# Performance work log

Hardware: AMD Instinct MI355X
Metric: run time of the kernel (lower is better)

The kernel has to match this reference:

```python
import jax, jax.numpy as jnp
import numpy as np

N = 100000      # spots (nodes)
E = 1600000     # directed edges
D_IN = 1000     # genes
ALPHA = 0.9
BN_EPS = 1e-3   # BatchNorm(momentum=0.01, eps=0.001), eval mode


def _bn(x, g, b, m, v):
    # eval-mode batchnorm with running stats
    return (x - m) * jax.lax.rsqrt(v + BN_EPS) * g + b


def _gcn(h, row, col, w, b):
    # PyG GCNConv: h' = D^-1/2 (A + I) D^-1/2 (h W) + b
    n = h.shape[0]
    h = h @ w
    ones = jnp.ones((row.shape[0],), h.dtype)
    deg = jnp.ones((n,), h.dtype).at[col].add(ones)  # degree incl. self-loop
    dinv = jax.lax.rsqrt(deg)
    msg = h[row] * (dinv[row] * dinv[col])[:, None]   # gather + edge norm
    agg = jnp.zeros_like(h).at[col].add(msg)          # scatter-add
    agg = agg + h * (1.0 / deg)[:, None]              # self-loop term
    return agg + b


def setup_inputs() -> dict:
    key = jax.random.key(0)
    ks = iter(jax.random.split(key, 48))
    f32 = jnp.float32

    def glorot(shape):
        return jax.random.normal(next(ks), shape, f32) * np.float32(1.0 / np.sqrt(shape[0]))

    def bnp(n):
        g = jax.random.uniform(next(ks), (n,), f32, 0.9, 1.1)
        b = jax.random.normal(next(ks), (n,), f32) * 0.1
        m = jax.random.normal(next(ks), (n,), f32) * 0.1
        v = jax.random.uniform(next(ks), (n,), f32, 0.5, 1.5)
        return g, b, m, v

    inp = {}
    inp['x'] = jax.random.normal(next(ks), (N, D_IN), f32)
    inp['edge_index'] = jax.random.randint(next(ks), (2, E), 0, N, jnp.int64)
    # encoder L0: 1000 -> 256
    inp['enc0_w'] = glorot((D_IN, 256)); inp['enc0_b'] = jnp.zeros((256,), f32)
    inp['enc0_g'], inp['enc0_bb'], inp['enc0_m'], inp['enc0_v'] = bnp(256)
    # encoder L1: 256 -> 64
    inp['enc1_w'] = glorot((256, 64)); inp['enc1_b'] = jnp.zeros((64,), f32)
    inp['enc1_g'], inp['enc1_bb'], inp['enc1_m'], inp['enc1_v'] = bnp(64)
    # GCN: 64 -> 128 (conv_hidden[0]*2)
    inp['conv_w'] = glorot((64, 128)); inp['conv_b'] = jnp.zeros((128,), f32)
    inp['conv_g'], inp['conv_bb'], inp['conv_m'], inp['conv_v'] = bnp(128)
    # GCN mean / logvar heads: 128 -> 16
    inp['mean_w'] = glorot((128, 16)); inp['mean_b'] = jnp.zeros((16,), f32)
    inp['logvar_w'] = glorot((128, 16)); inp['logvar_b'] = jnp.zeros((16,), f32)
    # decoder L0: 80 -> 64
    inp['dec0_w'] = glorot((80, 64)); inp['dec0_b'] = jnp.zeros((64,), f32)
    inp['dec0_g'], inp['dec0_bb'], inp['dec0_m'], inp['dec0_v'] = bnp(64)
    # decoder L1: 64 -> 1000
    inp['dec1_w'] = glorot((64, D_IN)); inp['dec1_b'] = jnp.zeros((D_IN,), f32)
    # cluster layer [15, 80]
    inp['cluster'] = jax.random.normal(next(ks), (15, 80), f32) * np.float32(np.sqrt(2.0 / (15 + 80)))
    return inp


def reference(x, edge_index, enc0_w, enc0_b, enc0_g, enc0_bb, enc0_m, enc0_v,
              enc1_w, enc1_b, enc1_g, enc1_bb, enc1_m, enc1_v,
              conv_w, conv_b, conv_g, conv_bb, conv_m, conv_v,
              mean_w, mean_b, logvar_w, logvar_b,
              dec0_w, dec0_b, dec0_g, dec0_bb, dec0_m, dec0_v,
              dec1_w, dec1_b, cluster):
    row, col = edge_index[0], edge_index[1]
    # linear encoder (Linear + BN(eval) + ELU; dropout off in eval)
    h = jax.nn.elu(_bn(x @ enc0_w + enc0_b, enc0_g, enc0_bb, enc0_m, enc0_v))
    feat_x = jax.nn.elu(_bn(h @ enc1_w + enc1_b, enc1_g, enc1_bb, enc1_m, enc1_v))
    # graph encoder
    c = jax.nn.relu(_bn(_gcn(feat_x, row, col, conv_w, conv_b), conv_g, conv_bb, conv_m, conv_v))
    mu = _gcn(c, row, col, mean_w, mean_b)
    logvar = _gcn(c, row, col, logvar_w, logvar_b)
    gnn_z = mu  # reparameterize in eval mode returns mu
    z = jnp.concatenate([feat_x, gnn_z], axis=1)  # [N, 80]
    # decoder
    d = jax.nn.elu(_bn(z @ dec0_w + dec0_b, dec0_g, dec0_bb, dec0_m, dec0_v))
    de_feat = d @ dec1_w + dec1_b
    # student-t cluster soft assignment (||z-c||^2 via expansion, no [N,K,80] tensor)
    dist = jnp.maximum(jnp.sum(z * z, 1, keepdims=True)
                       + jnp.sum(cluster * cluster, 1)[None, :]
                       - 2.0 * (z @ cluster.T), 0.0)
    q = 1.0 / (1.0 + dist / ALPHA + 1e-8)
    q = q ** ((ALPHA + 1.0) / 2.0)
    q = q / jnp.sum(q, 1, keepdims=True)
    return (z, mu, logvar, de_feat, q, feat_x, gnn_z)
```

## Files before the change

kernel.cpp:

```cpp
#include <hip/hip_runtime.h>
#include <hip/hip_bf16.h>

#define NN 100000
#define NE 1600000
#define DIN 1000
#define BN_EPS 1e-3f
#define NB 391

#define OZ  ((size_t)0)
#define OMU ((size_t)NN*80)
#define OLV ((size_t)NN*96)
#define ODE ((size_t)NN*112)
#define OQ  ((size_t)NN*1112)
#define OFX ((size_t)NN*1127)
#define OGZ ((size_t)NN*1191)

typedef __attribute__((ext_vector_type(8))) short short8v;
typedef __attribute__((ext_vector_type(4))) short short4v;
typedef __attribute__((ext_vector_type(4))) float f32x4;

__device__ __forceinline__ float elu_f(float x) { return x > 0.f ? x : expf(x) - 1.f; }

__device__ __forceinline__ short f2bf(float f) {
    union { float f; unsigned u; } c; c.f = f;
    unsigned r = c.u + 0x7fffu + ((c.u >> 16) & 1u);
    return (short)(r >> 16);
}
__device__ __forceinline__ float b2f(short s) {
    union { unsigned u; float f; } c; c.u = ((unsigned)(unsigned short)s) << 16; return c.f;
}
__device__ __forceinline__ float b2f_lo(unsigned p) {
    union { unsigned u; float f; } c; c.u = p << 16; return c.f;
}
__device__ __forceinline__ float b2f_hi(unsigned p) {
    union { unsigned u; float f; } c; c.u = p & 0xffff0000u; return c.f;
}

__device__ __forceinline__ int edge_at(const void* ei, int is64, size_t idx) {
    if (is64) return (int)((const long long*)ei)[idx];
    return ((const int*)ei)[idx];
}

__global__ __launch_bounds__(256) void k_detect(const int* __restrict__ ei, int* __restrict__ flag) {
    __shared__ int nz;
    if (threadIdx.x == 0) nz = 0;
    __syncthreads();
    for (int i = threadIdx.x; i < 2048; i += 256)
        if (ei[2 * i + 1] != 0) nz = 1;
    __syncthreads();
    if (threadIdx.x == 0) flag[0] = (nz == 0) ? 1 : 0;
}

__global__ __launch_bounds__(256) void k_deg_init(float* __restrict__ deg) {
    int i = blockIdx.x * 256 + threadIdx.x;
    if (i < NN) deg[i] = 1.0f;
}

__global__ __launch_bounds__(256) void k_deg_accum(const void* __restrict__ ei, const int* __restrict__ flag,
                                                   float* __restrict__ deg) {
    const int is64 = flag[0];
    int e = blockIdx.x * 256 + threadIdx.x;
    if (e < NE) atomicAdd(&deg[edge_at(ei, is64, (size_t)NE + e)], 1.0f);
}

__global__ __launch_bounds__(256) void k_scan1(const float* __restrict__ deg, int* __restrict__ off,
                                               int* __restrict__ bsum, int* __restrict__ cursor) {
    __shared__ int s[256];
    const int t = threadIdx.x;
    const int i = blockIdx.x * 256 + t;
    const int vv = (i < NN) ? ((int)deg[i]) - 1 : 0;
    if (i < NN) cursor[i] = 0;
    s[t] = vv;
    __syncthreads();
    for (int d = 1; d < 256; d <<= 1) {
        const int u = (t >= d) ? s[t - d] : 0;
        __syncthreads();
        s[t] += u;
        __syncthreads();
    }
    if (i < NN) off[i] = s[t] - vv;
    if (t == 255) bsum[blockIdx.x] = s[t];
}

__global__ __launch_bounds__(512) void k_scan2(int* __restrict__ bsum) {
    __shared__ int s[512];
    const int t = threadIdx.x;
    const int vv = (t < NB) ? bsum[t] : 0;
    s[t] = vv;
    __syncthreads();
    for (int d = 1; d < 512; d <<= 1) {
        const int u = (t >= d) ? s[t - d] : 0;
        __syncthreads();
        s[t] += u;
        __syncthreads();
    }
    if (t < NB) bsum[t] = s[t] - vv;
}

__global__ __launch_bounds__(256) void k_scan3(int* __restrict__ off, const int* __restrict__ bsum) {
    const int i = blockIdx.x * 256 + threadIdx.x;
    if (i < NN) off[i] += bsum[blockIdx.x];
}

__global__ __launch_bounds__(256) void k_fill(const void* __restrict__ ei, const int* __restrict__ flag,
                                              const float* __restrict__ deg, const int* __restrict__ off,
                                              int* __restrict__ cursor, int2* __restrict__ csr_e) {
    const int is64 = flag[0];
    const int e = blockIdx.x * 256 + threadIdx.x;
    if (e >= NE) return;
    const int r = edge_at(ei, is64, e);
    const int c = edge_at(ei, is64, (size_t)NE + e);
    const float w = rsqrtf(deg[r]) * rsqrtf(deg[c]);
    const int p = atomicAdd(&cursor[c], 1);
    csr_e[off[c] + p] = make_int2(r, __float_as_int(w));
}

__global__ __launch_bounds__(256) void k_wt(const float* __restrict__ w, short* __restrict__ wt) {
    const int tid = blockIdx.x * 256 + threadIdx.x;
    const int c = tid >> 10;
    const int k = tid & 1023;
    wt[((size_t)(k >> 3) * 256 + c) * 8 + (k & 7)] = (k < DIN) ? f2bf(w[(size_t)k * 256 + c]) : (short)0;
}

__global__ __launch_bounds__(256) void k_wt2(const float* __restrict__ w, short* __restrict__ wt2) {
    const int tid = blockIdx.x * 256 + threadIdx.x;
    const int c = tid >> 6;
    const int k = tid & 63;
    wt2[(size_t)c * 64 + k] = (c < DIN) ? f2bf(w[(size_t)k * DIN + c]) : (short)0;
}

__global__ __launch_bounds__(512, 2) void k_enc0_mfma(
    const float* __restrict__ x, const short* __restrict__ wt, const float* __restrict__ bias,
    const float* __restrict__ g, const float* __restrict__ bb,
    const float* __restrict__ m, const float* __restrict__ v,
    short* __restrict__ h1bf)
{
    __shared__ short As[4 * 128 * 8];
    __shared__ short Bs[4 * 256 * 8];
    const int t = threadIdx.x;
    const int lane = t & 63;
    const int wave = t >> 6;
    const int wm = (wave >> 2) * 64;
    const int wn = (wave & 3) * 64;
    const int row0 = blockIdx.x * 128;

    f32x4 acc[4][4];
    #pragma unroll
    for (int mi = 0; mi < 4; ++mi)
        #pragma unroll
        for (int ni = 0; ni < 4; ++ni)
            acc[mi][ni] = (f32x4){0.f, 0.f, 0.f, 0.f};

    const int kq = t & 7;
    const int rA0 = t >> 3;
    const int rA1 = rA0 + 64;
    const int gr0 = (row0 + rA0 < NN) ? (row0 + rA0) : (NN - 1);
    const int gr1 = (row0 + rA1 < NN) ? (row0 + rA1) : (NN - 1);
    const float* xb0 = x + (size_t)gr0 * DIN;
    const float* xb1 = x + (size_t)gr1 * DIN;
    short4v* aslot0 = reinterpret_cast<short4v*>(&As[(((kq >> 1) * 128) + rA0) * 8 + (kq & 1) * 4]);
    short4v* aslot1 = reinterpret_cast<short4v*>(&As[(((kq >> 1) * 128) + rA1) * 8 + (kq & 1) * 4]);

    const int colB = t & 255;
    const int kcB0 = t >> 8;
    const int kcB1 = 2 + (t >> 8);

    const int kc = lane >> 4;
    const int lr = lane & 15;

    float4 pf0 = *reinterpret_cast<const float4*>(xb0 + kq * 4);
    float4 pf1 = *reinterpret_cast<const float4*>(xb1 + kq * 4);

    for (int ks = 0; ks < 32; ++ks) {
        __syncthreads();
        {
            const int kb = ks * 32 + kq * 4;
            short4v p0, p1;
            if (kb + 4 <= DIN) {
                p0[0] = f2bf(pf0.x); p0[1] = f2bf(pf0.y); p0[2] = f2bf(pf0.z); p0[3] = f2bf(pf0.w);
                p1[0] = f2bf(pf1.x); p1[1] = f2bf(pf1.y); p1[2] = f2bf(pf1.z); p1[3] = f2bf(pf1.w);
            } else {
                p0 = (short4v){0, 0, 0, 0};
                p1 = (short4v){0, 0, 0, 0};
            }
            *aslot0 = p0;
            *aslot1 = p1;
        }
        {
            const int gbase = ks * 4;
            *reinterpret_cast<short8v*>(&Bs[((size_t)kcB0 * 256 + colB) * 8]) =
                *reinterpret_cast<const short8v*>(&wt[((size_t)(gbase + kcB0) * 256 + colB) * 8]);
            *reinterpret_cast<short8v*>(&Bs[((size_t)kcB1 * 256 + colB) * 8]) =
                *reinterpret_cast<const short8v*>(&wt[((size_t)(gbase + kcB1) * 256 + colB) * 8]);
        }
        if (ks + 1 < 32) {
            const int kb2 = (ks + 1) * 32 + kq * 4;
            const int ko = (kb2 + 4 <= DIN) ? kb2 : 0;
            pf0 = *reinterpret_cast<const float4*>(xb0 + ko);
            pf1 = *reinterpret_cast<const float4*>(xb1 + ko);
        }
        __syncthreads();
        short8v a[4], b[4];
        #pragma unroll
        for (int mi = 0; mi < 4; ++mi)
            a[mi] = *reinterpret_cast<const short8v*>(&As[((size_t)kc * 128 + wm + mi * 16 + lr) * 8]);
        #pragma unroll
        for (int ni = 0; ni < 4; ++ni)
            b[ni] = *reinterpret_cast<const short8v*>(&Bs[((size_t)kc * 256 + wn + ni * 16 + lr) * 8]);
        #pragma unroll
        for (int mi = 0; mi < 4; ++mi)
            #pragma unroll
            for (int ni = 0; ni < 4; ++ni)
                acc[mi][ni] = __builtin_amdgcn_mfma_f32_16x16x32_bf16(a[mi], b[ni], acc[mi][ni], 0, 0, 0);
    }

    float sc[4], sh[4];
    int cols[4];
    #pragma unroll
    for (int ni = 0; ni < 4; ++ni) {
        const int col = wn + ni * 16 + lr;
        cols[ni] = col;
        const float s = rsqrtf(v[col] + BN_EPS) * g[col];
        sc[ni] = s;
        sh[ni] = (bias[col] - m[col]) * s + bb[col];
    }
    #pragma unroll
    for (int mi = 0; mi < 4; ++mi) {
        #pragma unroll
        for (int j = 0; j < 4; ++j) {
            const int row = row0 + wm + mi * 16 + (lane >> 4) * 4 + j;
            if (row < NN) {
                #pragma unroll
                for (int ni = 0; ni < 4; ++ni) {
                    const float y = acc[mi][ni][j] * sc[ni] + sh[ni];
                    h1bf[(size_t)row * 256 + cols[ni]] = f2bf(elu_f(y));
                }
            }
        }
    }
}

__global__ __launch_bounds__(256) void k_enc1(
    const short* __restrict__ h1bf, const float* __restrict__ w, const float* __restrict__ bias,
    const float* __restrict__ g, const float* __restrict__ bb,
    const float* __restrict__ m, const float* __restrict__ v,
    float* __restrict__ feat, short* __restrict__ featbf, float* __restrict__ out)
{
    __shared__ short hs[32 * 256];
    const int t = threadIdx.x;
    const int row0 = blockIdx.x * 32;
    const int j0 = t & 31;
    const int r0 = (t >> 5) * 4;
    float acc[4][2] = {};
    for (int idx = t; idx < 1024; idx += 256) {
        const int r = idx >> 5, c8 = idx & 31;
        *reinterpret_cast<short8v*>(&hs[r * 256 + c8 * 8]) =
            *reinterpret_cast<const short8v*>(&h1bf[(size_t)(row0 + r) * 256 + c8 * 8]);
    }
    __syncthreads();
    #pragma unroll 1
    for (int k = 0; k < 256; k += 8) {
        float wv[8][2];
        #pragma unroll
        for (int kk = 0; kk < 8; ++kk) {
            wv[kk][0] = w[(k + kk) * 64 + j0];
            wv[kk][1] = w[(k + kk) * 64 + j0 + 32];
        }
        #pragma unroll
        for (int r = 0; r < 4; ++r) {
            const short8v hv = *reinterpret_cast<const short8v*>(&hs[(r0 + r) * 256 + k]);
            #pragma unroll
            for (int kk = 0; kk < 8; ++kk) {
                const float xa = b2f(hv[kk]);
                acc[r][0] = fmaf(xa, wv[kk][0], acc[r][0]);
                acc[r][1] = fmaf(xa, wv[kk][1], acc[r][1]);
            }
        }
    }
    #pragma unroll
    for (int c = 0; c < 2; ++c) {
        const int j = j0 + 32 * c;
        const float sc = rsqrtf(v[j] + BN_EPS) * g[j];
        const float sh = (bias[j] - m[j]) * sc + bb[j];
        #pragma unroll
        for (int r = 0; r < 4; ++r) {
            const size_t rowi = row0 + r0 + r;
            const float y = elu_f(acc[r][c] * sc + sh);
            feat[rowi * 64 + j] = y;
            featbf[rowi * 64 + j] = f2bf(y);
            out[OFX + rowi * 64 + j] = y;
            out[OZ + rowi * 80 + j] = y;
        }
    }
}

__global__ __launch_bounds__(256) void k_feat_gather(
    const unsigned* __restrict__ featp, const float* __restrict__ deg,
    const int* __restrict__ off, const int2* __restrict__ csr_e,
    float* __restrict__ aggF)
{
    const int t = threadIdx.x;
    const int node = blockIdx.x * 8 + (t >> 5);
    const int lane = t & 31;
    const float dg = deg[node];
    const float dinv = 1.0f / dg;
    const unsigned ps = featp[(size_t)node * 32 + lane];
    float a0 = b2f_lo(ps) * dinv;
    float a1 = b2f_hi(ps) * dinv;
    const int beg = off[node];
    const int end = beg + ((int)dg - 1);
    for (int s = beg; s < end; ++s) {
        const int2 e = csr_e[s];
        const float w = __int_as_float(e.y);
        const unsigned p = featp[(size_t)e.x * 32 + lane];
        a0 = fmaf(b2f_lo(p), w, a0);
        a1 = fmaf(b2f_hi(p), w, a1);
    }
    float2 o; o.x = a0; o.y = a1;
    *reinterpret_cast<float2*>(&aggF[(size_t)node * 64 + lane * 2]) = o;
}

__global__ __launch_bounds__(256) void k_conv_mlp_proj(
    const float* __restrict__ aggF, const float* __restrict__ w, const float* __restrict__ cb,
    const float* __restrict__ g, const float* __restrict__ bb,
    const float* __restrict__ m, const float* __restrict__ v,
    const float* __restrict__ mw, const float* __restrict__ lw,
    short* __restrict__ m2bf)
{
    __shared__ float fs[32 * 64];
    __shared__ float cs[32 * 128];
    const int t = threadIdx.x;
    const int row0 = blockIdx.x * 32;
    {
        const int j0 = t & 63;
        const int r0 = (t >> 6) * 8;
        float acc[8][2] = {};
        for (int idx = t; idx < 512; idx += 256) {
            const int r = idx >> 4, c4 = idx & 15;
            *reinterpret_cast<float4*>(&fs[r * 64 + c4 * 4]) =
                *reinterpret_cast<const float4*>(&aggF[(size_t)(row0 + r) * 64 + c4 * 4]);
        }
        __syncthreads();
        #pragma unroll 1
        for (int k = 0; k < 64; k += 4) {
            float wv[4][2];
            #pragma unroll
            for (int kk = 0; kk < 4; ++kk) {
                wv[kk][0] = w[(k + kk) * 128 + j0];
                wv[kk][1] = w[(k + kk) * 128 + j0 + 64];
            }
            #pragma unroll
            for (int r = 0; r < 8; ++r) {
                const float4 xv = *reinterpret_cast<const float4*>(&fs[(r0 + r) * 64 + k]);
                const float xa[4] = {xv.x, xv.y, xv.z, xv.w};
                #pragma unroll
                for (int kk = 0; kk < 4; ++kk) {
                    acc[r][0] = fmaf(xa[kk], wv[kk][0], acc[r][0]);
                    acc[r][1] = fmaf(xa[kk], wv[kk][1], acc[r][1]);
                }
            }
        }
        #pragma unroll
        for (int c = 0; c < 2; ++c) {
            const int j = j0 + 64 * c;
            const float sc = rsqrtf(v[j] + BN_EPS) * g[j];
            const float sh = bb[j] - m[j] * sc;
            const float cbj = cb[j];
            #pragma unroll
            for (int r = 0; r < 8; ++r) {
                const float val = acc[r][c] + cbj;
                cs[(r0 + r) * 128 + j] = fmaxf(fmaf(val, sc, sh), 0.f);
            }
        }
    }
    __syncthreads();
    {
        const int j0 = t & 15;
        const int r0 = (t >> 4) * 2;
        float acc[2][2] = {};
        #pragma unroll 1
        for (int k = 0; k < 128; k += 4) {
            float wv[4][2];
            #pragma unroll
            for (int kk = 0; kk < 4; ++kk) {
                wv[kk][0] = mw[(k + kk) * 16 + j0];
                wv[kk][1] = lw[(k + kk) * 16 + j0];
            }
            #pragma unroll
            for (int r = 0; r < 2; ++r) {
                const float4 xv = *reinterpret_cast<const float4*>(&cs[(r0 + r) * 128 + k]);
                const float xa[4] = {xv.x, xv.y, xv.z, xv.w};
                #pragma unroll
                for (int kk = 0; kk < 4; ++kk) {
                    acc[r][0] = fmaf(xa[kk], wv[kk][0], acc[r][0]);
                    acc[r][1] = fmaf(xa[kk], wv[kk][1], acc[r][1]);
                }
            }
        }
        #pragma unroll
        for (int r = 0; r < 2; ++r) {
            const size_t rowi = row0 + r0 + r;
            m2bf[rowi * 32 + j0] = f2bf(acc[r][0]);
            m2bf[rowi * 32 + 16 + j0] = f2bf(acc[r][1]);
        }
    }
}

__global__ __launch_bounds__(256) void k_mlp_gather(
    const unsigned* __restrict__ m2p, const float* __restrict__ deg,
    const int* __restrict__ off, const int2* __restrict__ csr_e,
    const float* __restrict__ mb, const float* __restrict__ lb,
    float* __restrict__ agg2)
{
    const int t = threadIdx.x;
    const int node = blockIdx.x * 16 + (t >> 4);
    const int lane = t & 15;
    const int f0 = lane * 2, f1 = lane * 2 + 1;
    const float dg = deg[node];
    const float dinv = 1.0f / dg;
    const float b0 = (f0 < 16) ? mb[f0] : lb[f0 - 16];
    const float b1 = (f1 < 16) ? mb[f1] : lb[f1 - 16];
    const unsigned ps = m2p[(size_t)node * 16 + lane];
    float a0 = fmaf(b2f_lo(ps), dinv, b0);
    float a1 = fmaf(b2f_hi(ps), dinv, b1);
    const int beg = off[node];
    const int end = beg + ((int)dg - 1);
    for (int s = beg; s < end; ++s) {
        const int2 e = csr_e[s];
        const float w = __int_as_float(e.y);
        const unsigned p = m2p[(size_t)e.x * 16 + lane];
        a0 = fmaf(b2f_lo(p), w, a0);
        a1 = fmaf(b2f_hi(p), w, a1);
    }
    float2 o; o.x = a0; o.y = a1;
    *reinterpret_cast<float2*>(&agg2[(size_t)node * 32 + lane * 2]) = o;
}

__global__ __launch_bounds__(256) void k_final_pre(
    const float* __restrict__ feat, const float* __restrict__ agg2,
    const float* __restrict__ d0w, const float* __restrict__ d0b,
    const float* __restrict__ g, const float* __restrict__ bb,
    const float* __restrict__ m, const float* __restrict__ v,
    const float* __restrict__ cluster,
    short* __restrict__ d0bf,
    float* __restrict__ out)
{
    __shared__ float zs[8][80];
    __shared__ float qs[8][15];
    const int t = threadIdx.x;
    const int row0 = blockIdx.x * 8;

    for (int idx = t; idx < 512; idx += 256) {
        const int r = idx >> 6, k = idx & 63;
        zs[r][k] = feat[(size_t)(row0 + r) * 64 + k];
    }
    if (t < 128) {
        const int r = t >> 4, k = t & 15;
        const size_t rowi = row0 + r;
        const float muv = agg2[rowi * 32 + k];
        const float lv = agg2[rowi * 32 + 16 + k];
        zs[r][64 + k] = muv;
        out[OMU + rowi * 16 + k] = muv;
        out[OGZ + rowi * 16 + k] = muv;
        out[OZ + rowi * 80 + 64 + k] = muv;
        out[OLV + rowi * 16 + k] = lv;
    }
    __syncthreads();

    for (int idx = t; idx < 512; idx += 256) {
        const int r = idx >> 6, n = idx & 63;
        float acc = 0.f;
        #pragma unroll
        for (int k = 0; k < 80; k += 4) {
            const float4 zv = *reinterpret_cast<const float4*>(&zs[r][k]);
            acc = fmaf(zv.x, d0w[(k + 0) * 64 + n], acc);
            acc = fmaf(zv.y, d0w[(k + 1) * 64 + n], acc);
            acc = fmaf(zv.z, d0w[(k + 2) * 64 + n], acc);
            acc = fmaf(zv.w, d0w[(k + 3) * 64 + n], acc);
        }
        acc += d0b[n];
        const float sc = rsqrtf(v[n] + BN_EPS) * g[n];
        const float y = elu_f((acc - m[n]) * sc + bb[n]);
        d0bf[(size_t)(row0 + r) * 64 + n] = f2bf(y);
    }

    if (t < 120) {
        const int r = t / 15, c = t % 15;
        float zz = 0.f, cc = 0.f, dot = 0.f;
        #pragma unroll 1
        for (int k = 0; k < 80; ++k) {
            const float zv = zs[r][k];
            const float cv = cluster[c * 80 + k];
            zz = fmaf(zv, zv, zz);
            cc = fmaf(cv, cv, cc);
            dot = fmaf(zv, cv, dot);
        }
        const float dist = fmaxf(zz + cc - 2.f * dot, 0.f);
        qs[r][c] = powf(1.0f / (1.0f + dist / 0.9f + 1e-8f), 0.95f);
    }
    __syncthreads();
    if (t < 120) {
        const int r = t / 15, c = t % 15;
        float s = 0.f;
        #pragma unroll
        for (int c2 = 0; c2 < 15; ++c2) s += qs[r][c2];
        out[OQ + (size_t)(row0 + r) * 15 + c] = qs[r][c] / s;
    }
}

__global__ __launch_bounds__(256) void k_dec1_mfma(
    const short* __restrict__ d0bf, const short* __restrict__ wt2,
    const float* __restrict__ d1b, float* __restrict__ out)
{
    const int t = threadIdx.x;
    const int lane = t & 63;
    const int wave = t >> 6;
    const int wm = (wave >> 1) * 64;
    const int wn = (wave & 1) * 64;
    const int row0 = blockIdx.x * 128;
    const int col0 = blockIdx.y * 128;
    const int kc = lane >> 4;
    const int lr = lane & 15;

    f32x4 acc[4][4];
    #pragma unroll
    for (int mi = 0; mi < 4; ++mi)
        #pragma unroll
        for (int ni = 0; ni < 4; ++ni)
            acc[mi][ni] = (f32x4){0.f, 0.f, 0.f, 0.f};

    #pragma unroll
    for (int ks = 0; ks < 2; ++ks) {
        const int k0 = ks * 32 + kc * 8;
        short8v a[4], b[4];
        #pragma unroll
        for (int mi = 0; mi < 4; ++mi) {
            const int row = row0 + wm + mi * 16 + lr;
            if (row < NN)
                a[mi] = *reinterpret_cast<const short8v*>(&d0bf[(size_t)row * 64 + k0]);
            else
                a[mi] = (short8v){0, 0, 0, 0, 0, 0, 0, 0};
        }
        #pragma unroll
        for (int ni = 0; ni < 4; ++ni) {
            const int col = col0 + wn + ni * 16 + lr;
            b[ni] = *reinterpret_cast<const short8v*>(&wt2[(size_t)col * 64 + k0]);
        }
        #pragma unroll
        for (int mi = 0; mi < 4; ++mi)
            #pragma unroll
            for (int ni = 0; ni < 4; ++ni)
                acc[mi][ni] = __builtin_amdgcn_mfma_f32_16x16x32_bf16(a[mi], b[ni], acc[mi][ni], 0, 0, 0);
    }

    #pragma unroll
    for (int ni = 0; ni < 4; ++ni) {
        const int col = col0 + wn + ni * 16 + lr;
        if (col < DIN) {
            const float bv = d1b[col];
            #pragma unroll
            for (int mi = 0; mi < 4; ++mi) {
                #pragma unroll
                for (int j = 0; j < 4; ++j) {
                    const int row = row0 + wm + mi * 16 + (lane >> 4) * 4 + j;
                    if (row < NN)
                        out[ODE + (size_t)row * DIN + col] = acc[mi][ni][j] + bv;
                }
            }
        }
    }
}

extern "C" void kernel_launch(void* const* d_in, const int* in_sizes, int n_in,
                              void* d_out, int out_size, void* d_ws, size_t ws_size,
                              hipStream_t stream)
{
    const float* x       = (const float*)d_in[0];
    const void*  ei      = d_in[1];
    const float* enc0_w  = (const float*)d_in[2];
    const float* enc0_b  = (const float*)d_in[3];
    const float* enc0_g  = (const float*)d_in[4];
    const float* enc0_bb = (const float*)d_in[5];
    const float* enc0_m  = (const float*)d_in[6];
    const float* enc0_v  = (const float*)d_in[7];
    const float* enc1_w  = (const float*)d_in[8];
    const float* enc1_b  = (const float*)d_in[9];
    const float* enc1_g  = (const float*)d_in[10];
    const float* enc1_bb = (const float*)d_in[11];
    const float* enc1_m  = (const float*)d_in[12];
    const float* enc1_v  = (const float*)d_in[13];
    const float* conv_w  = (const float*)d_in[14];
    const float* conv_b  = (const float*)d_in[15];
    const float* conv_g  = (const float*)d_in[16];
    const float* conv_bb = (const float*)d_in[17];
    const float* conv_m  = (const float*)d_in[18];
    const float* conv_v  = (const float*)d_in[19];
    const float* mean_w  = (const float*)d_in[20];
    const float* mean_b  = (const float*)d_in[21];
    const float* logvar_w = (const float*)d_in[22];
    const float* logvar_b = (const float*)d_in[23];
    const float* dec0_w  = (const float*)d_in[24];
    const float* dec0_b  = (const float*)d_in[25];
    const float* dec0_g  = (const float*)d_in[26];
    const float* dec0_bb = (const float*)d_in[27];
    const float* dec0_m  = (const float*)d_in[28];
    const float* dec0_v  = (const float*)d_in[29];
    const float* dec1_w  = (const float*)d_in[30];
    const float* dec1_b  = (const float*)d_in[31];
    const float* cluster = (const float*)d_in[32];

    float* ws = (float*)d_ws;
    float* deg  = ws;
    float* feat = ws + NN;
    float* A    = ws + (size_t)65 * NN;
    size_t base = (size_t)321 * NN;
    int*   off     = (int*)(ws + base);
    int*   cursor  = (int*)(ws + base + NN);
    int*   bsum    = (int*)(ws + base + 2 * (size_t)NN);
    int2*  csr_e   = (int2*)(ws + base + 2 * (size_t)NN + 512);
    short* wt      = (short*)(ws + base + 2 * (size_t)NN + 512 + 2 * (size_t)NE);
    int*   flag    = (int*)(ws + base + 2 * (size_t)NN + 512 + 2 * (size_t)NE + 131072);

    short* h1bf   = (short*)A;
    short* featbf = (short*)(A + (size_t)128 * NN);
    float* aggF   = A;
    short* m2bf   = (short*)(A + (size_t)128 * NN);
    float* agg2   = A + (size_t)32 * NN;
    short* d0bf   = (short*)(A + (size_t)64 * NN);
    short* wt2    = wt;

    float* out = (float*)d_out;

    k_detect<<<1, 256, 0, stream>>>((const int*)ei, flag);
    k_deg_init<<<NB, 256, 0, stream>>>(deg);
    k_deg_accum<<<NE / 256, 256, 0, stream>>>(ei, flag, deg);

    k_scan1<<<NB, 256, 0, stream>>>(deg, off, bsum, cursor);
    k_scan2<<<1, 512, 0, stream>>>(bsum);
    k_scan3<<<NB, 256, 0, stream>>>(off, bsum);
    k_fill<<<NE / 256, 256, 0, stream>>>(ei, flag, deg, off, cursor, csr_e);

    k_wt<<<1024, 256, 0, stream>>>(enc0_w, wt);
    k_enc0_mfma<<<(NN + 127) / 128, 512, 0, stream>>>(x, wt, enc0_b, enc0_g, enc0_bb, enc0_m, enc0_v, h1bf);
    k_wt2<<<256, 256, 0, stream>>>(dec1_w, wt2);

    k_enc1<<<NN / 32, 256, 0, stream>>>(h1bf, enc1_w, enc1_b, enc1_g, enc1_bb, enc1_m, enc1_v,
                                        feat, featbf, out);

    k_feat_gather<<<NN / 8, 256, 0, stream>>>((const unsigned*)featbf, deg, off, csr_e, aggF);
    k_conv_mlp_proj<<<NN / 32, 256, 0, stream>>>(aggF, conv_w, conv_b,
                                                 conv_g, conv_bb, conv_m, conv_v,
                                                 mean_w, logvar_w, m2bf);

    k_mlp_gather<<<NN / 16, 256, 0, stream>>>((const unsigned*)m2bf, deg, off, csr_e,
                                              mean_b, logvar_b, agg2);

    k_final_pre<<<NN / 8, 256, 0, stream>>>(feat, agg2, dec0_w, dec0_b, dec0_g, dec0_bb, dec0_m, dec0_v,
                                            cluster, d0bf, out);
    {
        dim3 grid((NN + 127) / 128, 8);
        k_dec1_mfma<<<grid, 256, 0, stream>>>(d0bf, wt2, dec1_b, out);
    }
}
```

Before: 1.053 ms.

## Double-buffer LDS tiles in encoder GEMM to overlap loads with MFMA

The encoder-0 bf16 MFMA GEMM now uses two LDS buffers for the A and B tiles. Global loads for the next K step, including the weight tile, are issued before the current step's MFMAs, and the results are written to the alternate buffer afterward, so only one barrier per iteration is needed. This is meant to hide global-memory latency behind compute and to remove one sync per K step. In exchange it doubles shared memory use (from 24KB to 48KB per block), which could limit occupancy at two blocks per CU, and it raises register pressure from the held prefetch values.

```diff
diff --git a/kernel.cpp b/kernel.cpp
--- a/kernel.cpp
+++ b/kernel.cpp
@@ -135,8 +135,8 @@
     const float* __restrict__ m, const float* __restrict__ v,
     short* __restrict__ h1bf)
 {
-    __shared__ short As[4 * 128 * 8];
-    __shared__ short Bs[4 * 256 * 8];
+    __shared__ short As[2][4 * 128 * 8];
+    __shared__ short Bs[2][4 * 256 * 8];
     const int t = threadIdx.x;
     const int lane = t & 63;
     const int wave = t >> 6;
@@ -158,60 +158,77 @@
     const int gr1 = (row0 + rA1 < NN) ? (row0 + rA1) : (NN - 1);
     const float* xb0 = x + (size_t)gr0 * DIN;
     const float* xb1 = x + (size_t)gr1 * DIN;
-    short4v* aslot0 = reinterpret_cast<short4v*>(&As[(((kq >> 1) * 128) + rA0) * 8 + (kq & 1) * 4]);
-    short4v* aslot1 = reinterpret_cast<short4v*>(&As[(((kq >> 1) * 128) + rA1) * 8 + (kq & 1) * 4]);
+    const size_t aoff0 = (((kq >> 1) * 128) + rA0) * 8 + (kq & 1) * 4;
+    const size_t aoff1 = (((kq >> 1) * 128) + rA1) * 8 + (kq & 1) * 4;
 
     const int colB = t & 255;
     const int kcB0 = t >> 8;
     const int kcB1 = 2 + (t >> 8);
+    const size_t boff0 = ((size_t)kcB0 * 256 + colB) * 8;
+    const size_t boff1 = ((size_t)kcB1 * 256 + colB) * 8;
 
     const int kc = lane >> 4;
     const int lr = lane & 15;
 
-    float4 pf0 = *reinterpret_cast<const float4*>(xb0 + kq * 4);
-    float4 pf1 = *reinterpret_cast<const float4*>(xb1 + kq * 4);
+    {
+        const float4 f0 = *reinterpret_cast<const float4*>(xb0 + kq * 4);
+        const float4 f1 = *reinterpret_cast<const float4*>(xb1 + kq * 4);
+        short4v p0, p1;
+        p0[0] = f2bf(f0.x); p0[1] = f2bf(f0.y); p0[2] = f2bf(f0.z); p0[3] = f2bf(f0.w);
+        p1[0] = f2bf(f1.x); p1[1] = f2bf(f1.y); p1[2] = f2bf(f1.z); p1[3] = f2bf(f1.w);
+        *reinterpret_cast<short4v*>(&As[0][aoff0]) = p0;
+        *reinterpret_cast<short4v*>(&As[0][aoff1]) = p1;
+        *reinterpret_cast<short8v*>(&Bs[0][boff0]) =
+            *reinterpret_cast<const short8v*>(&wt[((size_t)kcB0 * 256 + colB) * 8]);
+        *reinterpret_cast<short8v*>(&Bs[0][boff1]) =
+            *reinterpret_cast<const short8v*>(&wt[((size_t)kcB1 * 256 + colB) * 8]);
+    }
+    __syncthreads();
 
     for (int ks = 0; ks < 32; ++ks) {
-        __syncthreads();
-        {
-            const int kb = ks * 32 + kq * 4;
+        const int cur = ks & 1;
+        const int nxt = cur ^ 1;
+        float4 pf0, pf1;
+        short8v wb0, wb1;
+        const bool have_next = (ks + 1) < 32;
+        bool next_a_ok = false;
+        if (have_next) {
+            const int kb2 = (ks + 1) * 32 + kq * 4;
+            next_a_ok = (kb2 + 4 <= DIN);
+            const int ko = next_a_ok ? kb2 : 0;
+            pf0 = *reinterpret_cast<const float4*>(xb0 + ko);
+            pf1 = *reinterpret_cast<const float4*>(xb1 + ko);
+            const int gbase = (ks + 1) * 4;
+            wb0 = *reinterpret_cast<const short8v*>(&wt[((size_t)(gbase + kcB0) * 256 + colB) * 8]);
+            wb1 = *reinterpret_cast<const short8v*>(&wt[((size_t)(gbase + kcB1) * 256 + colB) * 8]);
+        }
+        short8v a[4], b[4];
+        #pragma unroll
+        for (int mi = 0; mi < 4; ++mi)
+            a[mi] = *reinterpret_cast<const short8v*>(&As[cur][((size_t)kc * 128 + wm + mi * 16 + lr) * 8]);
+        #pragma unroll
+        for (int ni = 0; ni < 4; ++ni)
+            b[ni] = *reinterpret_cast<const short8v*>(&Bs[cur][((size_t)kc * 256 + wn + ni * 16 + lr) * 8]);
+        #pragma unroll
+        for (int mi = 0; mi < 4; ++mi)
+            #pragma unroll
+            for (int ni = 0; ni < 4; ++ni)
+                acc[mi][ni] = __builtin_amdgcn_mfma_f32_16x16x32_bf16(a[mi], b[ni], acc[mi][ni], 0, 0, 0);
+        if (have_next) {
             short4v p0, p1;
-            if (kb + 4 <= DIN) {
+            if (next_a_ok) {
                 p0[0] = f2bf(pf0.x); p0[1] = f2bf(pf0.y); p0[2] = f2bf(pf0.z); p0[3] = f2bf(pf0.w);
                 p1[0] = f2bf(pf1.x); p1[1] = f2bf(pf1.y); p1[2] = f2bf(pf1.z); p1[3] = f2bf(pf1.w);
             } else {
                 p0 = (short4v){0, 0, 0, 0};
                 p1 = (short4v){0, 0, 0, 0};
             }
-            *aslot0 = p0;
-            *aslot1 = p1;
-        }
-        {
-            const int gbase = ks * 4;
-            *reinterpret_cast<short8v*>(&Bs[((size_t)kcB0 * 256 + colB) * 8]) =
-                *reinterpret_cast<const short8v*>(&wt[((size_t)(gbase + kcB0) * 256 + colB) * 8]);
-            *reinterpret_cast<short8v*>(&Bs[((size_t)kcB1 * 256 + colB) * 8]) =
-                *reinterpret_cast<const short8v*>(&wt[((size_t)(gbase + kcB1) * 256 + colB) * 8]);
-        }
-        if (ks + 1 < 32) {
-            const int kb2 = (ks + 1) * 32 + kq * 4;
-            const int ko = (kb2 + 4 <= DIN) ? kb2 : 0;
-            pf0 = *reinterpret_cast<const float4*>(xb0 + ko);
-            pf1 = *reinterpret_cast<const float4*>(xb1 + ko);
+            *reinterpret_cast<short4v*>(&As[nxt][aoff0]) = p0;
+            *reinterpret_cast<short4v*>(&As[nxt][aoff1]) = p1;
+            *reinterpret_cast<short8v*>(&Bs[nxt][boff0]) = wb0;
+            *reinterpret_cast<short8v*>(&Bs[nxt][boff1]) = wb1;
         }
         __syncthreads();
-        short8v a[4], b[4];
-        #pragma unroll
-        for (int mi = 0; mi < 4; ++mi)
-            a[mi] = *reinterpret_cast<const short8v*>(&As[((size_t)kc * 128 + wm + mi * 16 + lr) * 8]);
-        #pragma unroll
-        for (int ni = 0; ni < 4; ++ni)
-            b[ni] = *reinterpret_cast<const short8v*>(&Bs[((size_t)kc * 256 + wn + ni * 16 + lr) * 8]);
-        #pragma unroll
-        for (int mi = 0; mi < 4; ++mi)
-            #pragma unroll
-            for (int ni = 0; ni < 4; ++ni)
-                acc[mi][ni] = __builtin_amdgcn_mfma_f32_16x16x32_bf16(a[mi], b[ni], acc[mi][ni], 0, 0, 0);
     }
 
     float sc[4], sh[4];
```

Result: no change. 1.052 ms (-0.1%).
